# Kernel optimization log

Hardware: AMD Instinct MI355X
Metric: run time of the kernel (lower is better)

The kernel has to match this reference:

```python
import jax, jax.numpy as jnp
import numpy as np

N_NODES = 50000
N_EDGES = 1_600_000
HID = 64
BN_EPS = 1e-5


def setup_inputs() -> dict:
    key = jax.random.key(0)
    ks = jax.random.split(key, 16)
    x = jax.random.normal(ks[0], (N_NODES, 1), dtype=jnp.float32)
    edge_index = jax.random.randint(ks[1], (2, N_EDGES), 0, N_NODES, dtype=jnp.int32)
    s = 1.0 / np.sqrt(HID)
    # layer 1: 1 -> 64 -> 64
    w1a = jax.random.normal(ks[2], (1, HID), dtype=jnp.float32)
    b1a = jnp.zeros((HID,), jnp.float32)
    w2a = jax.random.normal(ks[3], (HID, HID), dtype=jnp.float32) * s
    b2a = jnp.zeros((HID,), jnp.float32)
    # layers 2-4 stacked: 64 -> 64 -> 64
    w1s = jax.random.normal(ks[4], (3, HID, HID), dtype=jnp.float32) * s
    b1s = jnp.zeros((3, HID), jnp.float32)
    w2s = jax.random.normal(ks[5], (3, HID, HID), dtype=jnp.float32) * s
    b2s = jnp.zeros((3, HID), jnp.float32)
    eps = jnp.zeros((4,), jnp.float32)  # train_eps=True, init 0
    gammas = jnp.ones((4, HID), jnp.float32)
    betas = jnp.zeros((4, HID), jnp.float32)
    fc_w = jax.random.normal(ks[6], (HID, 1), dtype=jnp.float32) * s
    fc_b = jnp.zeros((1,), jnp.float32)
    return {"x": x, "edge_index": edge_index, "w1a": w1a, "b1a": b1a,
            "w2a": w2a, "b2a": b2a, "w1s": w1s, "b1s": b1s, "w2s": w2s,
            "b2s": b2s, "eps": eps, "gammas": gammas, "betas": betas,
            "fc_w": fc_w, "fc_b": fc_b}


def _gin(h, src, dst, e, w1, b1, w2, b2):
    # sum_{j in N(i)} h_j  (messages from src, aggregated at dst)
    agg = jax.ops.segment_sum(h[src], dst, num_segments=N_NODES)
    z = (1.0 + e) * h + agg
    return jax.nn.relu(z @ w1 + b1) @ w2 + b2


def _bn(h, g, b):
    # BatchNorm1d, training mode: biased batch statistics over nodes
    mu = jnp.mean(h, axis=0)
    var = jnp.mean((h - mu) ** 2, axis=0)
    return (h - mu) * jax.lax.rsqrt(var + BN_EPS) * g + b


def reference(x, edge_index, w1a, b1a, w2a, b2a, w1s, b1s, w2s, b2s,
              eps, gammas, betas, fc_w, fc_b):
    src, dst = edge_index[0], edge_index[1]
    h = _bn(jax.nn.relu(_gin(x, src, dst, eps[0], w1a, b1a, w2a, b2a)),
            gammas[0], betas[0])
    for i in range(3):
        h = _bn(jax.nn.relu(_gin(h, src, dst, eps[i + 1],
                                 w1s[i], b1s[i], w2s[i], b2s[i])),
                gammas[i + 1], betas[i + 1])
    return h @ fc_w + fc_b
```

## Files before the change

### kernel.cpp

```cpp
#include <hip/hip_runtime.h>
#include <hip/hip_fp16.h>

#define HID 64
#define BN_EPS 1e-5f
#define WINSH 8
#define WINSZ 256
#define B1 256
#define PIT 72

typedef short bf16x8 __attribute__((ext_vector_type(8)));
typedef float f32x4 __attribute__((ext_vector_type(4)));

__device__ __forceinline__ unsigned short f2b(float f) {
    unsigned int u = __float_as_uint(f);
    u = (u + 0x7FFF + ((u >> 16) & 1)) >> 16;
    return (unsigned short)u;
}
__device__ __forceinline__ float b2f(unsigned short h) {
    return __uint_as_float(((unsigned int)h) << 16);
}
__device__ __forceinline__ f32x4 mfma_bf16(bf16x8 a, bf16x8 b, f32x4 c) {
    return __builtin_amdgcn_mfma_f32_16x16x32_bf16(a, b, c, 0, 0, 0);
}

__global__ __launch_bounds__(256) void prep_kernel(const float* __restrict__ w2a,
                                                   const float* __restrict__ w1s,
                                                   const float* __restrict__ w2s,
                                                   unsigned short* __restrict__ whi,
                                                   unsigned short* __restrict__ wlo,
                                                   float* __restrict__ stats,
                                                   const int* __restrict__ dst,
                                                   int* __restrict__ cnt,
                                                   int E, int nw, int chunk) {
    int blk = blockIdx.x, tid = threadIdx.x;
    if (blk < 7) {
        const float* srcm = (blk == 0) ? w2a : (blk <= 3 ? w1s + (size_t)(blk - 1) * 4096
                                                         : w2s + (size_t)(blk - 4) * 4096);
        unsigned short* dh = whi + (size_t)blk * 4096;
        unsigned short* dl = wlo + (size_t)blk * 4096;
        for (int idx = tid; idx < 4096; idx += 256) {
            int j = idx & 7;
            int lane = (idx >> 3) & 63;
            int ntkh = idx >> 9;
            int nt = ntkh >> 1, kh = ntkh & 1;
            int nc = nt * 16 + (lane & 15);
            int k = kh * 32 + (lane >> 4) * 8 + j;
            float v = srcm[k * 64 + nc];
            unsigned short h = f2b(v);
            dh[idx] = h;
            dl[idx] = f2b(v - b2f(h));
        }
    } else if (blk == 7) {
        stats[tid] = 0.f;
        stats[tid + 256] = 0.f;
    } else {
        __shared__ int c[256];
        int b = blk - 8;
        c[tid] = 0;
        __syncthreads();
        int lo = b * chunk;
        int hi = lo + chunk; if (hi > E) hi = E;
        if ((((size_t)(dst + lo)) & 15) == 0) {
            int n4 = (hi - lo) >> 2;
            const int4* d4p = (const int4*)(dst + lo);
            for (int g = tid; g < n4; g += 256) {
                int4 d4 = d4p[g];
                atomicAdd(&c[d4.x >> WINSH], 1);
                atomicAdd(&c[d4.y >> WINSH], 1);
                atomicAdd(&c[d4.z >> WINSH], 1);
                atomicAdd(&c[d4.w >> WINSH], 1);
            }
            for (int e = lo + (n4 << 2) + tid; e < hi; e += 256)
                atomicAdd(&c[dst[e] >> WINSH], 1);
        } else {
            for (int e = lo + tid; e < hi; e += 256) atomicAdd(&c[dst[e] >> WINSH], 1);
        }
        __syncthreads();
        if (tid < nw) cnt[tid * B1 + b] = c[tid];
    }
}

__global__ __launch_bounds__(256) void scan_a_kernel(const int* __restrict__ in,
                                                     int* __restrict__ partial,
                                                     int* __restrict__ blocksum, int n) {
    __shared__ int sums[256];
    int tid = threadIdx.x;
    int i = blockIdx.x * 256 + tid;
    int v = (i < n) ? in[i] : 0;
    sums[tid] = v;
    __syncthreads();
    for (int off = 1; off < 256; off <<= 1) {
        int t = (tid >= off) ? sums[tid - off] : 0;
        __syncthreads();
        sums[tid] += t;
        __syncthreads();
    }
    if (i < n) partial[i] = sums[tid] - v;
    if (tid == 255) blocksum[blockIdx.x] = sums[255];
}

__global__ __launch_bounds__(256) void scan_b_kernel(const int* __restrict__ blocksum,
                                                     int* __restrict__ blockoff, int nb) {
    __shared__ int s[256];
    __shared__ int carry;
    int tid = threadIdx.x;
    if (tid == 0) carry = 0;
    __syncthreads();
    for (int base = 0; base < nb; base += 256) {
        int i = base + tid;
        int v = (i < nb) ? blocksum[i] : 0;
        s[tid] = v;
        __syncthreads();
        for (int off = 1; off < 256; off <<= 1) {
            int t = (tid >= off) ? s[tid - off] : 0;
            __syncthreads();
            s[tid] += t;
            __syncthreads();
        }
        if (i < nb) blockoff[i] = carry + s[tid] - v;
        __syncthreads();
        if (tid == 0) carry += s[255];
        __syncthreads();
    }
}

__global__ __launch_bounds__(256) void p3_bucket_kernel(const int* __restrict__ src,
                                                        const int* __restrict__ dst,
                                                        const int* __restrict__ cpart,
                                                        const int* __restrict__ blockoff,
                                                        int* __restrict__ ebuf,
                                                        int E, int nw, int chunk) {
    __shared__ int cur[256];
    int tid = threadIdx.x, b = blockIdx.x;
    if (tid < nw) cur[tid] = cpart[tid * B1 + b] + blockoff[tid];
    __syncthreads();
    int lo = b * chunk;
    int hi = lo + chunk; if (hi > E) hi = E;
    if (((((size_t)(dst + lo)) | ((size_t)(src + lo))) & 15) == 0) {
        int n4 = (hi - lo) >> 2;
        const int4* d4p = (const int4*)(dst + lo);
        const int4* s4p = (const int4*)(src + lo);
        for (int g = tid; g < n4; g += 256) {
            int4 d4 = d4p[g];
            int4 s4 = s4p[g];
            int p0 = atomicAdd(&cur[d4.x >> WINSH], 1);
            ebuf[p0] = s4.x | ((d4.x & (WINSZ - 1)) << 24);
            int p1 = atomicAdd(&cur[d4.y >> WINSH], 1);
            ebuf[p1] = s4.y | ((d4.y & (WINSZ - 1)) << 24);
            int p2 = atomicAdd(&cur[d4.z >> WINSH], 1);
            ebuf[p2] = s4.z | ((d4.z & (WINSZ - 1)) << 24);
            int p3 = atomicAdd(&cur[d4.w >> WINSH], 1);
            ebuf[p3] = s4.w | ((d4.w & (WINSZ - 1)) << 24);
        }
        for (int e = lo + (n4 << 2) + tid; e < hi; e += 256) {
            int d = dst[e];
            int pos = atomicAdd(&cur[d >> WINSH], 1);
            ebuf[pos] = src[e] | ((d & (WINSZ - 1)) << 24);
        }
    } else {
        for (int e = lo + tid; e < hi; e += 256) {
            int d = dst[e];
            int pos = atomicAdd(&cur[d >> WINSH], 1);
            ebuf[pos] = src[e] | ((d & (WINSZ - 1)) << 24);
        }
    }
}

__global__ __launch_bounds__(256) void p4_fine_kernel(const int* __restrict__ ebuf,
                                                      const int* __restrict__ cpart,
                                                      const int* __restrict__ blockoff,
                                                      int* __restrict__ csr_src,
                                                      int* __restrict__ rowptr,
                                                      int* __restrict__ deg,
                                                      int E, int n, int nw) {
    __shared__ int fcnt[256];
    __shared__ int foff[256];
    int tid = threadIdx.x, w = blockIdx.x;
    int lo = cpart[w * B1] + blockoff[w];
    int hi = (w + 1 < nw) ? cpart[(w + 1) * B1] + blockoff[w + 1] : E;
    fcnt[tid] = 0;
    __syncthreads();
    for (int e = lo + tid; e < hi; e += 256) atomicAdd(&fcnt[(unsigned)ebuf[e] >> 24], 1);
    __syncthreads();
    int v = fcnt[tid];
    foff[tid] = v;
    __syncthreads();
    for (int off = 1; off < 256; off <<= 1) {
        int t = (tid >= off) ? foff[tid - off] : 0;
        __syncthreads();
        foff[tid] += t;
        __syncthreads();
    }
    int myoff = lo + foff[tid] - v;
    int node = w * WINSZ + tid;
    if (node < n) { rowptr[node] = myoff; deg[node] = v; }
    __syncthreads();
    fcnt[tid] = myoff;
    __syncthreads();
    for (int e = lo + tid; e < hi; e += 256) {
        int p = ebuf[e];
        int pos = atomicAdd(&fcnt[(unsigned)p >> 24], 1);
        csr_src[pos] = p & 0xFFFFFF;
    }
}

__global__ __launch_bounds__(256) void gather1_kernel(const float* __restrict__ x,
                                                      const int* __restrict__ rowptr,
                                                      const int* __restrict__ deg,
                                                      const int* __restrict__ csr_src,
                                                      const float* __restrict__ eps,
                                                      float* __restrict__ zscalar, int n) {
    int node = blockIdx.x * 4 + (threadIdx.x >> 6);
    int lane = threadIdx.x & 63;
    if (node >= n) return;
    int start = __builtin_amdgcn_readfirstlane(rowptr[node]);
    int cnt   = __builtin_amdgcn_readfirstlane(deg[node]);
    float a = 0.f;
    for (int i = lane; i < cnt; i += 64) a += x[csr_src[start + i]];
    for (int off = 32; off > 0; off >>= 1) a += __shfl_xor(a, off);
    if (lane == 0) zscalar[node] = (1.0f + eps[0]) * x[node] + a;
}

__global__ __launch_bounds__(256) void gatherz_kernel(const __half* __restrict__ hh16,
                                                      const float* __restrict__ stats_prev,
                                                      const float* __restrict__ gamma_prev,
                                                      const float* __restrict__ beta_prev,
                                                      const int* __restrict__ rowptr,
                                                      const int* __restrict__ deg,
                                                      const int* __restrict__ csr_src,
                                                      const float* __restrict__ eps,
                                                      int layer,
                                                      __half* __restrict__ zh16, int n) {
    int lane = threadIdx.x & 63;
    int half = lane >> 5;
    int fp = lane & 31;
    int node = blockIdx.x * 4 + (threadIdx.x >> 6);

    float inv_n = 1.0f / (float)n;
    float2 sm = ((const float2*)stats_prev)[fp];
    float2 sq = ((const float2*)(stats_prev + 64))[fp];
    float2 gm = ((const float2*)gamma_prev)[fp];
    float2 bt = ((const float2*)beta_prev)[fp];
    float mux = sm.x * inv_n, muy = sm.y * inv_n;
    float scx = gm.x * rsqrtf(sq.x * inv_n - mux * mux + BN_EPS);
    float scy = gm.y * rsqrtf(sq.y * inv_n - muy * muy + BN_EPS);
    float shx = bt.x - mux * scx;
    float shy = bt.y - muy * scy;

    if (node >= n) return;
    int start = __builtin_amdgcn_readfirstlane(rowptr[node]);
    int cnt   = __builtin_amdgcn_readfirstlane(deg[node]);

    const __half2* hh2 = (const __half2*)hh16;
    float ax0 = 0.f, ay0 = 0.f, ax1 = 0.f, ay1 = 0.f;
    float ax2 = 0.f, ay2 = 0.f, ax3 = 0.f, ay3 = 0.f;
    int e = 0;
    for (; e + 8 <= cnt; e += 8) {
        int s0 = csr_src[start + e + 0];
        int s1 = csr_src[start + e + 1];
        int s2 = csr_src[start + e + 2];
        int s3 = csr_src[start + e + 3];
        int s4 = csr_src[start + e + 4];
        int s5 = csr_src[start + e + 5];
        int s6 = csr_src[start + e + 6];
        int s7 = csr_src[start + e + 7];
        int r0 = half ? s1 : s0;
        int r1 = half ? s3 : s2;
        int r2 = half ? s5 : s4;
        int r3 = half ? s7 : s6;
        float2 v0 = __half22float2(hh2[(size_t)r0 * 32 + fp]);
        float2 v1 = __half22float2(hh2[(size_t)r1 * 32 + fp]);
        float2 v2 = __half22float2(hh2[(size_t)r2 * 32 + fp]);
        float2 v3 = __half22float2(hh2[(size_t)r3 * 32 + fp]);
        ax0 += v0.x; ay0 += v0.y;
        ax1 += v1.x; ay1 += v1.y;
        ax2 += v2.x; ay2 += v2.y;
        ax3 += v3.x; ay3 += v3.y;
    }
    for (; e < cnt; e += 2) {
        int idx = e + half;
        if (idx < cnt) {
            int s = csr_src[start + idx];
            float2 v = __half22float2(hh2[(size_t)s * 32 + fp]);
            ax0 += v.x; ay0 += v.y;
        }
    }
    float sx = (ax0 + ax1) + (ax2 + ax3);
    float sy = (ay0 + ay1) + (ay2 + ay3);
    sx += __shfl_xor(sx, 32);
    sy += __shfl_xor(sy, 32);

    float ep = 1.0f + eps[layer];
    float2 self = __half22float2(hh2[(size_t)node * 32 + fp]);
    float zx = fmaf(scx, fmaf(ep, self.x, sx), shx * (ep + (float)cnt));
    float zy = fmaf(scy, fmaf(ep, self.y, sy), shy * (ep + (float)cnt));
    if (half == 0) {
        ((__half2*)zh16)[(size_t)node * 32 + fp] = __floats2half2_rn(zx, zy);
    }
}

__global__ __launch_bounds__(256) void mlp_kernel(const __half* __restrict__ zh16,
                                                  const float* __restrict__ zscalar,
                                                  const float* __restrict__ w1a,
                                                  const float* __restrict__ b1a,
                                                  const unsigned short* __restrict__ w1h,
                                                  const unsigned short* __restrict__ w1l,
                                                  const float* __restrict__ b1v,
                                                  const unsigned short* __restrict__ w2h,
                                                  const unsigned short* __restrict__ w2l,
                                                  const float* __restrict__ b2v,
                                                  float* __restrict__ hpre,
                                                  __half* __restrict__ hh16,
                                                  float* __restrict__ stats,
                                                  int n, int mode,
                                                  int write_hpre, int write_hh) {
    __shared__ __align__(16) unsigned short Ah[64 * PIT];
    __shared__ __align__(16) unsigned short Al[64 * PIT];
    __shared__ float ssum[64], ssq[64];

    int tid = threadIdx.x;
    int base = blockIdx.x * 64;

    if (mode) {
        const unsigned int* z32 = (const unsigned int*)zh16;
        for (int i = tid; i < 2048; i += 256) {
            int nn = i >> 5, c = i & 31;
            unsigned int u = z32[(size_t)(base + nn) * 32 + c];
            __half2 hv = *(__half2*)&u;
            float vx = __half2float(hv.x);
            float vy = __half2float(hv.y);
            unsigned short hx = f2b(vx);
            unsigned short hy = f2b(vy);
            Ah[nn * PIT + 2 * c]     = hx;
            Ah[nn * PIT + 2 * c + 1] = hy;
            Al[nn * PIT + 2 * c]     = f2b(vx - b2f(hx));
            Al[nn * PIT + 2 * c + 1] = f2b(vy - b2f(hy));
        }
    } else {
        for (int i = tid; i < 4096; i += 256) {
            int nn = i >> 6, k = i & 63;
            float zv = zscalar[base + nn];
            float v = fmaxf(fmaf(zv, w1a[k], b1a[k]), 0.f);
            unsigned short h = f2b(v);
            Ah[nn * PIT + k] = h;
            Al[nn * PIT + k] = f2b(v - b2f(h));
        }
    }
    if (tid < 64) { ssum[tid] = 0.f; ssq[tid] = 0.f; }
    __syncthreads();

    int l = tid & 63;
    int m = l & 15;
    int q = l >> 4;
    int m0 = (tid >> 6) * 16;

    const bf16x8* a0h = (const bf16x8*)&Ah[(m0 + m) * PIT + q * 8];
    const bf16x8* a1h = (const bf16x8*)&Ah[(m0 + m) * PIT + 32 + q * 8];
    const bf16x8* a0l = (const bf16x8*)&Al[(m0 + m) * PIT + q * 8];
    const bf16x8* a1l = (const bf16x8*)&Al[(m0 + m) * PIT + 32 + q * 8];

    if (mode) {
        bf16x8 xa0h = *a0h, xa1h = *a1h, xa0l = *a0l, xa1l = *a1l;
        f32x4 acc[4];
#pragma unroll
        for (int nt = 0; nt < 4; ++nt) {
            size_t fo0 = ((size_t)(nt * 2 + 0) * 64 + l) * 8;
            size_t fo1 = ((size_t)(nt * 2 + 1) * 64 + l) * 8;
            bf16x8 b0h = *(const bf16x8*)(w1h + fo0);
            bf16x8 b1h_ = *(const bf16x8*)(w1h + fo1);
            bf16x8 b0l = *(const bf16x8*)(w1l + fo0);
            bf16x8 b1l_ = *(const bf16x8*)(w1l + fo1);
            f32x4 c = {0.f, 0.f, 0.f, 0.f};
            c = mfma_bf16(xa0h, b0h, c);
            c = mfma_bf16(xa0h, b0l, c);
            c = mfma_bf16(xa0l, b0h, c);
            c = mfma_bf16(xa1h, b1h_, c);
            c = mfma_bf16(xa1h, b1l_, c);
            c = mfma_bf16(xa1l, b1h_, c);
            acc[nt] = c;
        }
#pragma unroll
        for (int nt = 0; nt < 4; ++nt) {
            int col = nt * 16 + m;
            float bv = b1v[col];
#pragma unroll
            for (int r = 0; r < 4; ++r) {
                int row = m0 + q * 4 + r;
                float T = fmaxf(acc[nt][r] + bv, 0.f);
                unsigned short h = f2b(T);
                Ah[row * PIT + col] = h;
                Al[row * PIT + col] = f2b(T - b2f(h));
            }
        }
    }
    __syncthreads();

    {
        bf16x8 xa0h = *a0h, xa1h = *a1h, xa0l = *a0l, xa1l = *a1l;
        f32x4 acc[4];
#pragma unroll
        for (int nt = 0; nt < 4; ++nt) {
            size_t fo0 = ((size_t)(nt * 2 + 0) * 64 + l) * 8;
            size_t fo1 = ((size_t)(nt * 2 + 1) * 64 + l) * 8;
            bf16x8 b0h = *(const bf16x8*)(w2h + fo0);
            bf16x8 b1h_ = *(const bf16x8*)(w2h + fo1);
            bf16x8 b0l = *(const bf16x8*)(w2l + fo0);
            bf16x8 b1l_ = *(const bf16x8*)(w2l + fo1);
            f32x4 c = {0.f, 0.f, 0.f, 0.f};
            c = mfma_bf16(xa0h, b0h, c);
            c = mfma_bf16(xa0h, b0l, c);
            c = mfma_bf16(xa0l, b0h, c);
            c = mfma_bf16(xa1h, b1h_, c);
            c = mfma_bf16(xa1h, b1l_, c);
            c = mfma_bf16(xa1l, b1h_, c);
            acc[nt] = c;
        }
#pragma unroll
        for (int nt = 0; nt < 4; ++nt) {
            int col = nt * 16 + m;
            float bv = b2v[col];
            float cs = 0.f, cq = 0.f;
#pragma unroll
            for (int r = 0; r < 4; ++r) {
                int node = base + m0 + q * 4 + r;
                float h = fmaxf(acc[nt][r] + bv, 0.f);
                if (node < n) {
                    if (write_hpre) hpre[(size_t)node * HID + col] = h;
                    if (write_hh) hh16[(size_t)node * HID + col] = __float2half(h);
                    cs += h;
                    cq = fmaf(h, h, cq);
                }
            }
            cs += __shfl_xor(cs, 16); cs += __shfl_xor(cs, 32);
            cq += __shfl_xor(cq, 16); cq += __shfl_xor(cq, 32);
            if (q == 0) {
                atomicAdd(&ssum[col], cs);
                atomicAdd(&ssq[col], cq);
            }
        }
    }
    __syncthreads();
    if (tid < 64) {
        atomicAdd(&stats[tid], ssum[tid]);
        atomicAdd(&stats[64 + tid], ssq[tid]);
    }
}

__global__ __launch_bounds__(256) void final_kernel(const float* __restrict__ hpre,
                                                    const float* __restrict__ stats,
                                                    const float* __restrict__ gamma,
                                                    const float* __restrict__ beta,
                                                    const float* __restrict__ fcw,
                                                    const float* __restrict__ fcb,
                                                    float* __restrict__ out, int n) {
    int wave = threadIdx.x >> 6;
    int lane = threadIdx.x & 63;
    int node = blockIdx.x * 4 + wave;
    if (node < n) {
        float inv_n = 1.0f / (float)n;
        float mu = stats[lane] * inv_n;
        float var = stats[64 + lane] * inv_n - mu * mu;
        float inv = rsqrtf(var + BN_EPS);
        float sc = gamma[lane] * inv;
        float sh = beta[lane] - mu * sc;
        float v = hpre[(size_t)node * HID + lane];
        float t = fmaf(v, sc, sh) * fcw[lane];
        for (int off = 32; off > 0; off >>= 1) t += __shfl_xor(t, off);
        if (lane == 0) out[node] = t + fcb[0];
    }
}

extern "C" void kernel_launch(void* const* d_in, const int* in_sizes, int n_in,
                              void* d_out, int out_size, void* d_ws, size_t ws_size,
                              hipStream_t stream) {
    const float* x      = (const float*)d_in[0];
    const int*   ei     = (const int*)d_in[1];
    const float* w1a    = (const float*)d_in[2];
    const float* b1a    = (const float*)d_in[3];
    const float* w2a    = (const float*)d_in[4];
    const float* b2a    = (const float*)d_in[5];
    const float* w1s    = (const float*)d_in[6];
    const float* b1s    = (const float*)d_in[7];
    const float* w2s    = (const float*)d_in[8];
    const float* b2s    = (const float*)d_in[9];
    const float* eps    = (const float*)d_in[10];
    const float* gammas = (const float*)d_in[11];
    const float* betas  = (const float*)d_in[12];
    const float* fcw    = (const float*)d_in[13];
    const float* fcb    = (const float*)d_in[14];
    float* out = (float*)d_out;

    int n = in_sizes[0];
    int E = in_sizes[1] / 2;
    int npad = ((n + 63) / 64) * 64;
    int nblk = npad / 64;

    int nw = (n + WINSZ - 1) >> WINSH;
    int NWB = nw * B1;
    int chunk = (((E + B1 - 1) / B1) + 3) & ~3;
    int nbs2 = (NWB + 255) / 256;

    const int* src = ei;
    const int* dst = ei + E;

    char* p = (char*)d_ws;
    float* csrtmp  = (float*)p; p += (size_t)npad * HID * 4;
    float* hpre    = (float*)p; p += (size_t)npad * HID * 4;
    __half* hh16   = (__half*)p; p += (size_t)npad * HID * 2;
    __half* zh16   = (__half*)p; p += (size_t)npad * HID * 2;
    float* zscalar = (float*)p; p += (size_t)npad * 4;
    float* stats   = (float*)p; p += 4 * 128 * 4;
    unsigned short* whi = (unsigned short*)p; p += 7 * 4096 * 2;
    unsigned short* wlo = (unsigned short*)p; p += 7 * 4096 * 2;
    int* deg     = (int*)p; p += (size_t)n * 4;
    int* rowptr  = (int*)p; p += (size_t)n * 4;
    int* csr_src = (int*)p; p += (size_t)E * 4;

    int* ebuf     = (int*)csrtmp;
    int* cnt      = ebuf + E;
    int* cpart    = cnt + NWB;
    int* bsum     = cpart + NWB;
    int* blockoff = bsum + nbs2;

    prep_kernel<<<8 + B1, 256, 0, stream>>>(w2a, w1s, w2s, whi, wlo, stats,
                                            dst, cnt, E, nw, chunk);
    scan_a_kernel<<<nbs2, 256, 0, stream>>>(cnt, cpart, bsum, NWB);
    scan_b_kernel<<<1, 256, 0, stream>>>(bsum, blockoff, nbs2);
    p3_bucket_kernel<<<B1, 256, 0, stream>>>(src, dst, cpart, blockoff, ebuf, E, nw, chunk);
    p4_fine_kernel<<<nw, 256, 0, stream>>>(ebuf, cpart, blockoff, csr_src, rowptr, deg,
                                           E, n, nw);

    gather1_kernel<<<(n + 3) / 4, 256, 0, stream>>>(x, rowptr, deg, csr_src, eps, zscalar, n);
    mlp_kernel<<<nblk, 256, 0, stream>>>(zh16, zscalar, w1a, b1a,
                                         whi, wlo, b1a ,
                                         whi , wlo, b2a,
                                         hpre, hh16, stats, n, 0,
                                         0, 1);

    for (int l = 1; l <= 3; ++l) {
        gatherz_kernel<<<(n + 3) / 4, 256, 0, stream>>>(hh16,
                                                        stats + (l - 1) * 128,
                                                        gammas + (l - 1) * HID,
                                                        betas + (l - 1) * HID,
                                                        rowptr, deg, csr_src, eps, l, zh16, n);
        mlp_kernel<<<nblk, 256, 0, stream>>>(zh16, zscalar, w1a, b1a,
                                             whi + (size_t)l * 4096,
                                             wlo + (size_t)l * 4096,
                                             b1s + (size_t)(l - 1) * HID,
                                             whi + (size_t)(3 + l) * 4096,
                                             wlo + (size_t)(3 + l) * 4096,
                                             b2s + (size_t)(l - 1) * HID,
                                             hpre, hh16, stats + l * 128,
                                             n, 1,
                                             (l == 3) ? 1 : 0,
                                             (l < 3) ? 1 : 0);
    }
    final_kernel<<<(n + 3) / 4, 256, 0, stream>>>(hpre, stats + 3 * 128,
                                                  gammas + 3 * HID, betas + 3 * HID,
                                                  fcw, fcb, out, n);
}
```

Before: 378.4 us.

## Split fp16 hidden features into two column halves for cache-resident gathers

The MLP kernel now writes the fp16 hidden state as two separate 32-column planes, and each layer's neighbour gather runs as two launches, one per plane, with 16 lanes per row and 4 edges in flight per wavefront. Each gather pass touches a 3.2 MB table instead of 6.4 MB, so the random row reads are meant to hit the L2/MALL cache more often. The cost is reading the CSR indices and rowptr/deg twice per layer, one extra launch per layer, and 64-byte row reads that may use memory transactions less efficiently.

```diff
diff --git a/kernel.cpp b/kernel.cpp
--- a/kernel.cpp
+++ b/kernel.cpp
@@ -221,7 +221,7 @@
     if (lane == 0) zscalar[node] = (1.0f + eps[0]) * x[node] + a;
 }
 
-__global__ __launch_bounds__(256) void gatherz_kernel(const __half* __restrict__ hh16,
+__global__ __launch_bounds__(256) void gatherz_kernel(const __half* __restrict__ T,
                                                       const float* __restrict__ stats_prev,
                                                       const float* __restrict__ gamma_prev,
                                                       const float* __restrict__ beta_prev,
@@ -229,18 +229,19 @@
                                                       const int* __restrict__ deg,
                                                       const int* __restrict__ csr_src,
                                                       const float* __restrict__ eps,
-                                                      int layer,
+                                                      int layer, int p,
                                                       __half* __restrict__ zh16, int n) {
     int lane = threadIdx.x & 63;
-    int half = lane >> 5;
-    int fp = lane & 31;
+    int es = lane >> 4;
+    int fp = lane & 15;
     int node = blockIdx.x * 4 + (threadIdx.x >> 6);
 
+    int gfp = p * 16 + fp;
     float inv_n = 1.0f / (float)n;
-    float2 sm = ((const float2*)stats_prev)[fp];
-    float2 sq = ((const float2*)(stats_prev + 64))[fp];
-    float2 gm = ((const float2*)gamma_prev)[fp];
-    float2 bt = ((const float2*)beta_prev)[fp];
+    float2 sm = ((const float2*)stats_prev)[gfp];
+    float2 sq = ((const float2*)(stats_prev + 64))[gfp];
+    float2 gm = ((const float2*)gamma_prev)[gfp];
+    float2 bt = ((const float2*)beta_prev)[gfp];
     float mux = sm.x * inv_n, muy = sm.y * inv_n;
     float scx = gm.x * rsqrtf(sq.x * inv_n - mux * mux + BN_EPS);
     float scy = gm.y * rsqrtf(sq.y * inv_n - muy * muy + BN_EPS);
@@ -251,51 +252,41 @@
     int start = __builtin_amdgcn_readfirstlane(rowptr[node]);
     int cnt   = __builtin_amdgcn_readfirstlane(deg[node]);
 
-    const __half2* hh2 = (const __half2*)hh16;
+    const __half2* T2 = (const __half2*)T;
     float ax0 = 0.f, ay0 = 0.f, ax1 = 0.f, ay1 = 0.f;
     float ax2 = 0.f, ay2 = 0.f, ax3 = 0.f, ay3 = 0.f;
     int e = 0;
-    for (; e + 8 <= cnt; e += 8) {
-        int s0 = csr_src[start + e + 0];
-        int s1 = csr_src[start + e + 1];
-        int s2 = csr_src[start + e + 2];
-        int s3 = csr_src[start + e + 3];
-        int s4 = csr_src[start + e + 4];
-        int s5 = csr_src[start + e + 5];
-        int s6 = csr_src[start + e + 6];
-        int s7 = csr_src[start + e + 7];
-        int r0 = half ? s1 : s0;
-        int r1 = half ? s3 : s2;
-        int r2 = half ? s5 : s4;
-        int r3 = half ? s7 : s6;
-        float2 v0 = __half22float2(hh2[(size_t)r0 * 32 + fp]);
-        float2 v1 = __half22float2(hh2[(size_t)r1 * 32 + fp]);
-        float2 v2 = __half22float2(hh2[(size_t)r2 * 32 + fp]);
-        float2 v3 = __half22float2(hh2[(size_t)r3 * 32 + fp]);
+    for (; e + 16 <= cnt; e += 16) {
+        int i0 = start + e + es;
+        int s0 = csr_src[i0];
+        int s1 = csr_src[i0 + 4];
+        int s2 = csr_src[i0 + 8];
+        int s3 = csr_src[i0 + 12];
+        float2 v0 = __half22float2(T2[(size_t)s0 * 16 + fp]);
+        float2 v1 = __half22float2(T2[(size_t)s1 * 16 + fp]);
+        float2 v2 = __half22float2(T2[(size_t)s2 * 16 + fp]);
+        float2 v3 = __half22float2(T2[(size_t)s3 * 16 + fp]);
         ax0 += v0.x; ay0 += v0.y;
         ax1 += v1.x; ay1 += v1.y;
         ax2 += v2.x; ay2 += v2.y;
         ax3 += v3.x; ay3 += v3.y;
     }
-    for (; e < cnt; e += 2) {
-        int idx = e + half;
-        if (idx < cnt) {
-            int s = csr_src[start + idx];
-            float2 v = __half22float2(hh2[(size_t)s * 32 + fp]);
-            ax0 += v.x; ay0 += v.y;
-        }
+    for (int i = e + es; i < cnt; i += 4) {
+        int s = csr_src[start + i];
+        float2 v = __half22float2(T2[(size_t)s * 16 + fp]);
+        ax0 += v.x; ay0 += v.y;
     }
     float sx = (ax0 + ax1) + (ax2 + ax3);
     float sy = (ay0 + ay1) + (ay2 + ay3);
-    sx += __shfl_xor(sx, 32);
-    sy += __shfl_xor(sy, 32);
+    sx += __shfl_xor(sx, 16); sx += __shfl_xor(sx, 32);
+    sy += __shfl_xor(sy, 16); sy += __shfl_xor(sy, 32);
 
     float ep = 1.0f + eps[layer];
-    float2 self = __half22float2(hh2[(size_t)node * 32 + fp]);
+    float2 self = __half22float2(T2[(size_t)node * 16 + fp]);
     float zx = fmaf(scx, fmaf(ep, self.x, sx), shx * (ep + (float)cnt));
     float zy = fmaf(scy, fmaf(ep, self.y, sy), shy * (ep + (float)cnt));
-    if (half == 0) {
-        ((__half2*)zh16)[(size_t)node * 32 + fp] = __floats2half2_rn(zx, zy);
+    if (es == 0) {
+        ((__half2*)zh16)[(size_t)node * 32 + p * 16 + fp] = __floats2half2_rn(zx, zy);
     }
 }
 
@@ -310,7 +301,8 @@
                                                   const unsigned short* __restrict__ w2l,
                                                   const float* __restrict__ b2v,
                                                   float* __restrict__ hpre,
-                                                  __half* __restrict__ hh16,
+                                                  __half* __restrict__ hhA,
+                                                  __half* __restrict__ hhB,
                                                   float* __restrict__ stats,
                                                   int n, int mode,
                                                   int write_hpre, int write_hh) {
@@ -426,7 +418,10 @@
                 float h = fmaxf(acc[nt][r] + bv, 0.f);
                 if (node < n) {
                     if (write_hpre) hpre[(size_t)node * HID + col] = h;
-                    if (write_hh) hh16[(size_t)node * HID + col] = __float2half(h);
+                    if (write_hh) {
+                        __half* ht = (nt < 2) ? hhA : hhB;
+                        ht[(size_t)node * 32 + (col & 31)] = __float2half(h);
+                    }
                     cs += h;
                     cq = fmaf(h, h, cq);
                 }
@@ -506,7 +501,8 @@
     char* p = (char*)d_ws;
     float* csrtmp  = (float*)p; p += (size_t)npad * HID * 4;
     float* hpre    = (float*)p; p += (size_t)npad * HID * 4;
-    __half* hh16   = (__half*)p; p += (size_t)npad * HID * 2;
+    __half* hhA    = (__half*)p; p += (size_t)npad * 32 * 2;
+    __half* hhB    = (__half*)p; p += (size_t)npad * 32 * 2;
     __half* zh16   = (__half*)p; p += (size_t)npad * HID * 2;
     float* zscalar = (float*)p; p += (size_t)npad * 4;
     float* stats   = (float*)p; p += 4 * 128 * 4;
@@ -534,15 +530,20 @@
     mlp_kernel<<<nblk, 256, 0, stream>>>(zh16, zscalar, w1a, b1a,
                                          whi, wlo, b1a ,
                                          whi , wlo, b2a,
-                                         hpre, hh16, stats, n, 0,
+                                         hpre, hhA, hhB, stats, n, 0,
                                          0, 1);
 
     for (int l = 1; l <= 3; ++l) {
-        gatherz_kernel<<<(n + 3) / 4, 256, 0, stream>>>(hh16,
+        gatherz_kernel<<<(n + 3) / 4, 256, 0, stream>>>(hhA,
                                                         stats + (l - 1) * 128,
                                                         gammas + (l - 1) * HID,
                                                         betas + (l - 1) * HID,
-                                                        rowptr, deg, csr_src, eps, l, zh16, n);
+                                                        rowptr, deg, csr_src, eps, l, 0, zh16, n);
+        gatherz_kernel<<<(n + 3) / 4, 256, 0, stream>>>(hhB,
+                                                        stats + (l - 1) * 128,
+                                                        gammas + (l - 1) * HID,
+                                                        betas + (l - 1) * HID,
+                                                        rowptr, deg, csr_src, eps, l, 1, zh16, n);
         mlp_kernel<<<nblk, 256, 0, stream>>>(zh16, zscalar, w1a, b1a,
                                              whi + (size_t)l * 4096,
                                              wlo + (size_t)l * 4096,
@@ -550,7 +551,7 @@
                                              whi + (size_t)(3 + l) * 4096,
                                              wlo + (size_t)(3 + l) * 4096,
                                              b2s + (size_t)(l - 1) * HID,
-                                             hpre, hh16, stats + l * 128,
+                                             hpre, hhA, hhB, stats + l * 128,
                                              n, 1,
                                              (l == 3) ? 1 : 0,
                                              (l < 3) ? 1 : 0);
```

New measurement: 432.9 us. 1.14x slower.
